# Optimization experiments

Hardware: AMD Instinct MI355X
Metric: run time of the kernel (lower is better)

The kernel has to match this reference:

```python
import math
import jax, jax.numpy as jnp
import numpy as np

NUM_HEADS = 16
INPUT_DIM = 1024
VALUES_DIM = 1024
HEAD_DIM = INPUT_DIM // NUM_HEADS


def _pos_embeddings(length, dim):
    # TENER positional encoding for `length` positions centered at 0: [length, dim]
    half = dim // 2
    position = jnp.arange(-(length // 2), length // 2, dtype=jnp.float32)[:, None]
    div_term = jnp.exp(jnp.arange(half, dtype=jnp.float32) * (-math.log(10000.0) / (half - 1)))
    ang = position * div_term[None, :]
    return jnp.concatenate([jnp.sin(ang), jnp.cos(ang)], axis=1)


def _shift(t):
    # [B,H,S,2S] -> [B,H,S,S] relative-position shift trick
    B, H, S, _ = t.shape
    t = jnp.concatenate([t, jnp.zeros((B, H, S, 1), t.dtype)], axis=-1)  # [B,H,S,2S+1]
    t = t.reshape(B, H, 2 * S + 1, S)[:, :, :-1].reshape(B, H, S, 2 * S)
    return t[..., S:]


def setup_inputs() -> dict:
    key = jax.random.key(0)
    ks = jax.random.split(key, 9)
    B, S, D, Dv = 2, 1024, INPUT_DIM, VALUES_DIM
    s = 1.0 / math.sqrt(D)
    return {
        "query": jax.random.normal(ks[0], (B, S, D), jnp.float32),
        "key": jax.random.normal(ks[1], (B, S, D), jnp.float32),
        "value": jax.random.normal(ks[2], (B, S, D), jnp.float32),
        "mask": jnp.ones((B, S), jnp.int32),
        "Wq": jax.random.normal(ks[3], (D, D), jnp.float32) * s,
        "bq": jnp.zeros((D,), jnp.float32),
        "Wv": jax.random.normal(ks[4], (Dv, D), jnp.float32) * s,
        "bv": jnp.zeros((Dv,), jnp.float32),
        "Wo": jax.random.normal(ks[5], (D, Dv), jnp.float32) * (1.0 / math.sqrt(Dv)),
        "bo": jnp.zeros((D,), jnp.float32),
        "v_bias": jax.random.normal(ks[6], (NUM_HEADS, HEAD_DIM), jnp.float32) * (1.0 / math.sqrt(HEAD_DIM)),
    }


def reference(query, key, value, mask, Wq, bq, Wv, bv, Wo, bo, v_bias):
    B, S, D = query.shape
    H, d = NUM_HEADS, HEAD_DIM
    dv = VALUES_DIM // H
    pos = _pos_embeddings(2 * S, d)  # [2S, d]

    k = key.reshape(B, S, H, d).transpose(0, 2, 1, 3)                       # [B,H,S,d] (no projection!)
    q = (query @ Wq.T + bq).reshape(B, S, H, d).transpose(0, 2, 1, 3)       # [B,H,S,d]
    v = (value @ Wv.T + bv).reshape(B, S, H, dv).transpose(0, 2, 1, 3)      # [B,H,S,dv]

    qk = jnp.einsum('bhqd,bhkd->bhqk', q, k)                                # [B,H,S,S]
    v_bias_rel = jnp.einsum('hd,ld->hl', v_bias, pos)[None, :, None, :]     # [1,H,1,2S]
    q_rel = jnp.einsum('bhqd,ld->bhql', q, pos)                             # [B,H,S,2S]
    rel = _shift(q_rel + v_bias_rel)                                        # [B,H,S,S]

    attn = jax.nn.softmax(qk + rel, axis=-1)                                # unscaled, unmasked (matches source)
    x = jnp.einsum('bhqk,bhkd->bhqd', attn, v)                              # [B,H,S,dv]
    x = x.transpose(0, 2, 1, 3).reshape(B, S, VALUES_DIM)
    return x @ Wo.T + bo
```

## Files before the change

### kernel.cpp

```cpp
#include <hip/hip_runtime.h>
#include <math.h>

#define SEQ 1024
#define DIM 1024
#define NH 16
#define HD 64
#define NB 2

typedef __attribute__((ext_vector_type(8))) short bf16x8;
typedef __attribute__((ext_vector_type(8))) _Float16 f16x8;
typedef __attribute__((ext_vector_type(4))) float f32x4;
typedef __attribute__((ext_vector_type(8))) unsigned short ushort8;
typedef __attribute__((ext_vector_type(4))) unsigned short ushort4v;

#define DT_CONST (-0.2971077539347156f)
#define FIXEDM 32.0f

__device__ __forceinline__ unsigned short f2bf(float x) {
    unsigned u = __float_as_uint(x);
    return (unsigned short)((u + 0x7fffu + ((u >> 16) & 1u)) >> 16);
}
__device__ __forceinline__ float bf2f(unsigned short h) {
    return __uint_as_float(((unsigned)h) << 16);
}
__device__ __forceinline__ unsigned short f2h(float x) {
    _Float16 h = (_Float16)x;
    return __builtin_bit_cast(unsigned short, h);
}

__device__ __forceinline__ void plain8(const float* __restrict__ s,
                                       unsigned short* __restrict__ h, int i) {
    float4 v0 = *(const float4*)&s[i];
    float4 v1 = *(const float4*)&s[i + 4];
    float vs[8] = {v0.x, v0.y, v0.z, v0.w, v1.x, v1.y, v1.z, v1.w};
    ushort8 hv;
    #pragma unroll
    for (int k = 0; k < 8; ++k) hv[k] = f2bf(vs[k]);
    *(ushort8*)&h[i] = hv;
}
__device__ __forceinline__ void plain8h(const float* __restrict__ s,
                                        unsigned short* __restrict__ h, int i) {
    float4 v0 = *(const float4*)&s[i];
    float4 v1 = *(const float4*)&s[i + 4];
    float vs[8] = {v0.x, v0.y, v0.z, v0.w, v1.x, v1.y, v1.z, v1.w};
    ushort8 hv;
    #pragma unroll
    for (int k = 0; k < 8; ++k) hv[k] = f2h(vs[k]);
    *(ushort8*)&h[i] = hv;
}

__global__ __launch_bounds__(256) void conv_all(
    const float* __restrict__ query, const float* __restrict__ key,
    const float* __restrict__ value, const float* __restrict__ Wq,
    const float* __restrict__ Wv, const float* __restrict__ Wo,
    unsigned short* __restrict__ Aqh,
    unsigned short* __restrict__ Khs,
    unsigned short* __restrict__ Vb,
    unsigned short* __restrict__ Wqh,
    unsigned short* __restrict__ Wvh,
    unsigned short* __restrict__ Woh,
    unsigned short* __restrict__ Kth)
{
    int i = (blockIdx.x * 256 + threadIdx.x) * 8;
    int r = blockIdx.y;
    const int NSMALL = DIM * DIM;
    if (r >= 3 && r <= 5 && i >= NSMALL) return;
    if (r == 6 && i >= SEQ * HD) return;
    switch (r) {
        case 0: plain8h(query, Aqh, i); break;
        case 1: plain8h(key,   Khs, i); break;
        case 2: plain8(value, Vb, i); break;
        case 3: plain8h(Wq, Wqh, i); break;
        case 4: plain8(Wv, Wvh, i); break;
        case 5: plain8(Wo, Woh, i); break;
        case 6: {
            ushort8 hv;
            #pragma unroll
            for (int k = 0; k < 8; ++k) {
                int idx = i + k;
                int j = idx >> 6;
                int c = idx & 63;
                int ii = c & 31;
                float dt = __expf((float)ii * DT_CONST);
                float ang = (float)j * dt;
                float val = (c < 32) ? sinf(ang) : cosf(ang);
                hv[k] = f2h(val);
            }
            *(ushort8*)&Kth[i] = hv;
            break;
        }
    }
}

#define QLD 72

__global__ __launch_bounds__(256) void qv_gemm(
    const unsigned short* __restrict__ Aqh, const unsigned short* __restrict__ Wqh,
    const float* __restrict__ bq,
    const unsigned short* __restrict__ Vb, const unsigned short* __restrict__ Wvh,
    const float* __restrict__ bv,
    const float* __restrict__ v_bias,
    unsigned short* __restrict__ Qh,
    unsigned short* __restrict__ vpT)
{
    __shared__ __align__(16) unsigned short smem[192 * QLD];
    unsigned short* sAh = smem;
    unsigned short* sWh = smem + 128 * QLD;

    const int K = DIM;

    int bid = blockIdx.x;
    int s = bid >> 3;
    int y = (bid & 7) + 8 * (s & 1);
    int h = (s >> 1) & 15;
    bool isq = (s >> 5) == 0;
    int m0 = y * 128;
    int n0 = h * 64;

    int tid = threadIdx.x;
    int lane = tid & 63;
    int w = tid >> 6;
    int l16 = lane & 15, quad = lane >> 4;

    int ar = tid >> 2;
    int c0 = (tid & 3) << 3;
    int c1 = c0 + 32;

    const unsigned short* pAh0 = (isq ? Aqh : Vb) + (size_t)(m0 + ar) * K;
    const unsigned short* pAh1 = pAh0 + (size_t)64 * K;
    const unsigned short* pWh  = (isq ? Wqh : Wvh) + (size_t)(n0 + ar) * K;

    f32x4 acc[2][4];
    #pragma unroll
    for (int mq = 0; mq < 2; ++mq)
        #pragma unroll
        for (int nt = 0; nt < 4; ++nt)
            acc[mq][nt] = (f32x4){0.f, 0.f, 0.f, 0.f};

    ushort8 ra[4], rw[2];
    ra[0] = *(const ushort8*)(pAh0 + c0);  ra[1] = *(const ushort8*)(pAh0 + c1);
    ra[2] = *(const ushort8*)(pAh1 + c0);  ra[3] = *(const ushort8*)(pAh1 + c1);
    rw[0] = *(const ushort8*)(pWh + c0);   rw[1] = *(const ushort8*)(pWh + c1);

    for (int kk = 0; kk < K; kk += 64) {
        __syncthreads();
        *(ushort8*)&sAh[ar * QLD + c0] = ra[0];
        *(ushort8*)&sAh[ar * QLD + c1] = ra[1];
        *(ushort8*)&sAh[(ar + 64) * QLD + c0] = ra[2];
        *(ushort8*)&sAh[(ar + 64) * QLD + c1] = ra[3];
        *(ushort8*)&sWh[ar * QLD + c0] = rw[0];
        *(ushort8*)&sWh[ar * QLD + c1] = rw[1];
        if (kk + 64 < K) {
            int kn = kk + 64;
            ra[0] = *(const ushort8*)(pAh0 + kn + c0);  ra[1] = *(const ushort8*)(pAh0 + kn + c1);
            ra[2] = *(const ushort8*)(pAh1 + kn + c0);  ra[3] = *(const ushort8*)(pAh1 + kn + c1);
            rw[0] = *(const ushort8*)(pWh + kn + c0);   rw[1] = *(const ushort8*)(pWh + kn + c1);
        }
        __syncthreads();

        #pragma unroll
        for (int c = 0; c < 2; ++c) {
            int kpos = c * 32 + quad * 8;
            bf16x8 af[2];
            #pragma unroll
            for (int mq = 0; mq < 2; ++mq)
                af[mq] = *(const bf16x8*)&sAh[(w * 32 + mq * 16 + l16) * QLD + kpos];
            bf16x8 bhv[4];
            #pragma unroll
            for (int nt = 0; nt < 4; ++nt)
                bhv[nt] = *(const bf16x8*)&sWh[(nt * 16 + l16) * QLD + kpos];
            if (isq) {
                #pragma unroll
                for (int nt = 0; nt < 4; ++nt)
                    #pragma unroll
                    for (int mq = 0; mq < 2; ++mq)
                        acc[mq][nt] = __builtin_amdgcn_mfma_f32_16x16x32_f16(
                            __builtin_bit_cast(f16x8, af[mq]),
                            __builtin_bit_cast(f16x8, bhv[nt]), acc[mq][nt], 0, 0, 0);
            } else {
                #pragma unroll
                for (int nt = 0; nt < 4; ++nt)
                    #pragma unroll
                    for (int mq = 0; mq < 2; ++mq)
                        acc[mq][nt] = __builtin_amdgcn_mfma_f32_16x16x32_bf16(
                            af[mq], bhv[nt], acc[mq][nt], 0, 0, 0);
            }
        }
    }

    int b = m0 >> 10;

    if (isq) {
        float bql[4], vbs[2], vbc[2], dti[2];
        #pragma unroll
        for (int nt = 0; nt < 4; ++nt) bql[nt] = bq[h * 64 + nt * 16 + l16];
        #pragma unroll
        for (int t = 0; t < 2; ++t) {
            vbs[t] = v_bias[h * 64 + t * 16 + l16];
            vbc[t] = v_bias[h * 64 + 32 + t * 16 + l16];
            dti[t] = __expf((float)(t * 16 + l16) * DT_CONST);
        }
        #pragma unroll
        for (int mq = 0; mq < 2; ++mq) {
            #pragma unroll
            for (int reg = 0; reg < 4; ++reg) {
                int row = m0 + w * 32 + mq * 16 + quad * 4 + reg;
                int q = row & (SEQ - 1);
                size_t qbase = ((size_t)(b * NH + h) * SEQ + q) * 128;
                float hv[4];
                #pragma unroll
                for (int nt = 0; nt < 4; ++nt) hv[nt] = acc[mq][nt][reg] + bql[nt];
                #pragma unroll
                for (int nt = 0; nt < 4; ++nt)
                    Qh[qbase + nt * 16 + l16] = f2h(hv[nt]);
                #pragma unroll
                for (int t = 0; t < 2; ++t) {
                    float u = hv[t] + vbs[t];
                    float wv = hv[t + 2] + vbc[t];
                    float ang = (float)q * dti[t];
                    float C = cosf(ang), S = sinf(ang);
                    float cs = u * C + wv * S;
                    float cc = wv * C - u * S;
                    Qh[qbase + 64 + t * 16 + l16] = f2h(cs);
                    Qh[qbase + 96 + t * 16 + l16] = f2h(cc);
                }
            }
        }
    } else {
        __syncthreads();
        unsigned short* tb = smem;
        #pragma unroll
        for (int nt = 0; nt < 4; ++nt) {
            int d = nt * 16 + l16;
            float bcol = bv[n0 + d];
            #pragma unroll
            for (int mq = 0; mq < 2; ++mq)
                #pragma unroll
                for (int reg = 0; reg < 4; ++reg) {
                    int srow = w * 32 + mq * 16 + quad * 4 + reg;
                    tb[d * 136 + srow] = f2bf(acc[mq][nt][reg] + bcol);
                }
        }
        __syncthreads();
        int s0 = m0 & (SEQ - 1);
        #pragma unroll
        for (int i = tid; i < 1024; i += 256) {
            int dd = i >> 4;
            int j16 = i & 15;
            int sb = j16 >> 3;
            int posl = (j16 & 7) << 3;
            unsigned short tmp[8];
            #pragma unroll
            for (int k = 0; k < 8; ++k) {
                int pos = posl + k;
                int sl = (pos >> 2) + (pos & 3) * 16;
                tmp[k] = tb[dd * 136 + sb * 64 + sl];
            }
            *(ushort8*)&vpT[((size_t)((b * NH + h) * 64 + dd)) * SEQ + s0 + sb * 64 + posl] =
                *(ushort8*)tmp;
        }
    }
}

__global__ __launch_bounds__(256) void out_gemm(
    const unsigned short* __restrict__ Ab, const unsigned short* __restrict__ Woh,
    const float* __restrict__ bo, float* __restrict__ C)
{
    __shared__ __align__(16) unsigned short sA[64 * QLD];
    __shared__ __align__(16) unsigned short sW[64 * QLD];

    const int K = DIM, N = DIM;

    int bid = blockIdx.x;
    int n0 = ((bid >> 3) & 15) * 64;
    int m0 = ((bid & 7) + 8 * (bid >> 7)) * 64;

    int tid = threadIdx.x;
    int lane = tid & 63;
    int w = tid >> 6;
    int l16 = lane & 15, quad = lane >> 4;

    int ar = tid >> 2;
    int c0 = (tid & 3) << 3;
    int c1 = c0 + 32;

    const unsigned short* pA = Ab + (size_t)(m0 + ar) * K;
    const unsigned short* pW = Woh + (size_t)(n0 + ar) * K;

    f32x4 acc[4];
    #pragma unroll
    for (int nt = 0; nt < 4; ++nt) acc[nt] = (f32x4){0.f, 0.f, 0.f, 0.f};

    ushort8 ra[2], rw[2];
    ra[0] = *(const ushort8*)(pA + c0);  ra[1] = *(const ushort8*)(pA + c1);
    rw[0] = *(const ushort8*)(pW + c0);  rw[1] = *(const ushort8*)(pW + c1);

    for (int kk = 0; kk < K; kk += 64) {
        __syncthreads();
        *(ushort8*)&sA[ar * QLD + c0] = ra[0];
        *(ushort8*)&sA[ar * QLD + c1] = ra[1];
        *(ushort8*)&sW[ar * QLD + c0] = rw[0];
        *(ushort8*)&sW[ar * QLD + c1] = rw[1];
        if (kk + 64 < K) {
            int kn = kk + 64;
            ra[0] = *(const ushort8*)(pA + kn + c0);  ra[1] = *(const ushort8*)(pA + kn + c1);
            rw[0] = *(const ushort8*)(pW + kn + c0);  rw[1] = *(const ushort8*)(pW + kn + c1);
        }
        __syncthreads();

        #pragma unroll
        for (int c = 0; c < 2; ++c) {
            int kpos = c * 32 + quad * 8;
            bf16x8 af = *(const bf16x8*)&sA[(w * 16 + l16) * QLD + kpos];
            #pragma unroll
            for (int nt = 0; nt < 4; ++nt) {
                bf16x8 bh = *(const bf16x8*)&sW[(nt * 16 + l16) * QLD + kpos];
                acc[nt] = __builtin_amdgcn_mfma_f32_16x16x32_bf16(af, bh, acc[nt], 0, 0, 0);
            }
        }
    }

    #pragma unroll
    for (int nt = 0; nt < 4; ++nt) {
        int col = n0 + nt * 16 + l16;
        float bcol = bo[col];
        #pragma unroll
        for (int reg = 0; reg < 4; ++reg) {
            int row = m0 + w * 16 + quad * 4 + reg;
            C[(size_t)row * N + col] = acc[nt][reg] + bcol;
        }
    }
}

#define LDK 136
#define LDV 72

__global__ __launch_bounds__(256) void attn_mfma(
    const unsigned short* __restrict__ Kh,
    const unsigned short* __restrict__ vpT,
    const unsigned short* __restrict__ Qh,
    const unsigned short* __restrict__ Kth,
    unsigned short* __restrict__ Opart,
    float* __restrict__ lsum)
{
    __shared__ unsigned short Ksh[64][LDK];
    __shared__ unsigned short Vt[64][LDV];
    __shared__ unsigned short Ps[128][LDV];

    int tid = threadIdx.x;
    int w = tid >> 6;
    int lane = tid & 63;
    int l16 = lane & 15;
    int quad = lane >> 4;

    int bid = blockIdx.x;
    int g = bid & 63;
    int qt = bid >> 6;
    int h = g & 15;
    int b = (g >> 4) & 1;
    int sp = g >> 5;
    int q0 = qt << 7;
    int jb = sp << 3;

    int sr0 = tid >> 3, sp0 = (tid & 7) << 3;
    int sr1 = sr0 + 32;

    ushort8 pK0, pK1, pT0, pT1, pV0, pV1;
    {
        int j0 = jb << 6;
        size_t g0 = (size_t)(b * SEQ + j0 + sr0) * DIM + h * HD + sp0;
        size_t g1 = (size_t)(b * SEQ + j0 + sr1) * DIM + h * HD + sp0;
        pK0 = *(const ushort8*)&Kh[g0]; pK1 = *(const ushort8*)&Kh[g1];
        size_t t0 = (size_t)(j0 + sr0) * 64 + sp0, t1 = (size_t)(j0 + sr1) * 64 + sp0;
        pT0 = *(const ushort8*)&Kth[t0]; pT1 = *(const ushort8*)&Kth[t1];
        size_t v0 = ((size_t)((b * NH + h) * 64 + sr0)) * SEQ + j0 + sp0;
        size_t v1 = ((size_t)((b * NH + h) * 64 + sr1)) * SEQ + j0 + sp0;
        pV0 = *(const ushort8*)&vpT[v0]; pV1 = *(const ushort8*)&vpT[v1];
    }

    bf16x8 ah[2][4];
    #pragma unroll
    for (int half = 0; half < 2; ++half) {
        const unsigned short* gq = Qh + (((size_t)(b * NH + h)) * SEQ + q0 + half * 64) * 128;
        #pragma unroll
        for (int c = tid; c < 1024; c += 256) {
            int r = c >> 4, p = (c & 15) << 3;
            *(ushort8*)&Ksh[r][p] = *(const ushort8*)&gq[r * 128 + p];
        }
        __syncthreads();
        if ((w >> 1) == half) {
            #pragma unroll
            for (int mq = 0; mq < 2; ++mq)
                #pragma unroll
                for (int c = 0; c < 4; ++c)
                    ah[mq][c] = *(const bf16x8*)&Ksh[(w & 1) * 32 + mq * 16 + l16][c * 32 + quad * 8];
        }
        __syncthreads();
    }

    f32x4 oacc[2][4];
    f32x4 lacc[2];
    #pragma unroll
    for (int mq = 0; mq < 2; ++mq) {
        #pragma unroll
        for (int nb = 0; nb < 4; ++nb) oacc[mq][nb] = (f32x4){0.f, 0.f, 0.f, 0.f};
        lacc[mq] = (f32x4){0.f, 0.f, 0.f, 0.f};
    }

    bf16x8 onesv;
    #pragma unroll
    for (int k = 0; k < 8; ++k) onesv[k] = (short)0x3F80;

    for (int jt = 0; jt < 8; ++jt) {
        __syncthreads();
        *(ushort8*)&Ksh[sr0][sp0] = pK0;       *(ushort8*)&Ksh[sr1][sp0] = pK1;
        *(ushort8*)&Ksh[sr0][64 + sp0] = pT0;  *(ushort8*)&Ksh[sr1][64 + sp0] = pT1;
        *(ushort8*)&Vt[sr0][sp0] = pV0;        *(ushort8*)&Vt[sr1][sp0] = pV1;
        if (jt < 7) {
            int j0n = (jb + jt + 1) << 6;
            size_t g0 = (size_t)(b * SEQ + j0n + sr0) * DIM + h * HD + sp0;
            size_t g1 = (size_t)(b * SEQ + j0n + sr1) * DIM + h * HD + sp0;
            pK0 = *(const ushort8*)&Kh[g0]; pK1 = *(const ushort8*)&Kh[g1];
            size_t t0 = (size_t)(j0n + sr0) * 64 + sp0, t1 = (size_t)(j0n + sr1) * 64 + sp0;
            pT0 = *(const ushort8*)&Kth[t0]; pT1 = *(const ushort8*)&Kth[t1];
            size_t v0 = ((size_t)((b * NH + h) * 64 + sr0)) * SEQ + j0n + sp0;
            size_t v1 = ((size_t)((b * NH + h) * 64 + sr1)) * SEQ + j0n + sp0;
            pV0 = *(const ushort8*)&vpT[v0]; pV1 = *(const ushort8*)&vpT[v1];
        }
        __syncthreads();

        f32x4 sacc[2][4];
        #pragma unroll
        for (int mq = 0; mq < 2; ++mq)
            #pragma unroll
            for (int nb = 0; nb < 4; ++nb) sacc[mq][nb] = (f32x4){0.f, 0.f, 0.f, 0.f};
        #pragma unroll
        for (int nb = 0; nb < 4; ++nb) {
            #pragma unroll
            for (int c = 0; c < 4; ++c) {
                bf16x8 bh = *(const bf16x8*)&Ksh[nb * 16 + l16][c * 32 + quad * 8];
                #pragma unroll
                for (int mq = 0; mq < 2; ++mq)
                    sacc[mq][nb] = __builtin_amdgcn_mfma_f32_16x16x32_f16(
                        __builtin_bit_cast(f16x8, ah[mq][c]),
                        __builtin_bit_cast(f16x8, bh), sacc[mq][nb], 0, 0, 0);
            }
        }

        #pragma unroll
        for (int mq = 0; mq < 2; ++mq) {
            #pragma unroll
            for (int r = 0; r < 4; ++r) {
                float p0 = __expf(sacc[mq][0][r] - FIXEDM);
                float p1 = __expf(sacc[mq][1][r] - FIXEDM);
                float p2 = __expf(sacc[mq][2][r] - FIXEDM);
                float p3 = __expf(sacc[mq][3][r] - FIXEDM);
                int prow = w * 32 + mq * 16 + quad * 4 + r;
                ushort4v pv4;
                pv4.x = f2bf(p0); pv4.y = f2bf(p1); pv4.z = f2bf(p2); pv4.w = f2bf(p3);
                *(ushort4v*)&Ps[prow][l16 * 4] = pv4;
            }
        }
        __syncthreads();

        #pragma unroll
        for (int kc = 0; kc < 2; ++kc) {
            bf16x8 a[2];
            #pragma unroll
            for (int mq = 0; mq < 2; ++mq) {
                a[mq] = *(const bf16x8*)&Ps[w * 32 + mq * 16 + l16][kc * 32 + quad * 8];
                lacc[mq] = __builtin_amdgcn_mfma_f32_16x16x32_bf16(a[mq], onesv, lacc[mq], 0, 0, 0);
            }
            #pragma unroll
            for (int nb = 0; nb < 4; ++nb) {
                bf16x8 bv = *(const bf16x8*)&Vt[nb * 16 + l16][kc * 32 + quad * 8];
                #pragma unroll
                for (int mq = 0; mq < 2; ++mq)
                    oacc[mq][nb] = __builtin_amdgcn_mfma_f32_16x16x32_bf16(a[mq], bv, oacc[mq][nb], 0, 0, 0);
            }
        }
    }

    const size_t OOFF = (size_t)sp * NB * NH * SEQ * 64;
    const size_t LOFF = (size_t)sp * NB * NH * SEQ;
    #pragma unroll
    for (int mq = 0; mq < 2; ++mq) {
        #pragma unroll
        for (int r = 0; r < 4; ++r) {
            int qrow = q0 + w * 32 + mq * 16 + quad * 4 + r;
            size_t rowi = (size_t)(b * NH + h) * SEQ + qrow;
            #pragma unroll
            for (int nb = 0; nb < 4; ++nb)
                Opart[OOFF + rowi * 64 + nb * 16 + l16] = f2bf(oacc[mq][nb][r]);
            if (l16 == 0)
                lsum[LOFF + rowi] = lacc[mq][r];
        }
    }
}

__global__ __launch_bounds__(256) void attn_combine(
    const unsigned short* __restrict__ Opart, const float* __restrict__ lsum,
    unsigned short* __restrict__ xab)
{
    const size_t OOFF = (size_t)NB * NH * SEQ * 64;
    const size_t LOFF = (size_t)NB * NH * SEQ;
    int tid = threadIdx.x;
    int d = tid & 63;
    size_t r = (size_t)blockIdx.x * 4 + (tid >> 6);
    int q = (int)(r & (SEQ - 1));
    int h = (int)((r >> 10) & (NH - 1));
    int b = (int)(r >> 14);

    float inv = 1.f / (lsum[r] + lsum[LOFF + r]);
    float O0 = bf2f(Opart[r * 64 + d]);
    float O1 = bf2f(Opart[OOFF + r * 64 + d]);
    float o = (O0 + O1) * inv;
    xab[((size_t)(b * SEQ + q)) * DIM + h * HD + d] = f2bf(o);
}

extern "C" void kernel_launch(void* const* d_in, const int* in_sizes, int n_in,
                              void* d_out, int out_size, void* d_ws, size_t ws_size,
                              hipStream_t stream) {
    const float* query  = (const float*)d_in[0];
    const float* key    = (const float*)d_in[1];
    const float* value  = (const float*)d_in[2];
    const float* Wq     = (const float*)d_in[4];
    const float* bq     = (const float*)d_in[5];
    const float* Wv     = (const float*)d_in[6];
    const float* bv     = (const float*)d_in[7];
    const float* Wo     = (const float*)d_in[8];
    const float* bo     = (const float*)d_in[9];
    const float* v_bias = (const float*)d_in[10];

    float* out = (float*)d_out;
    char* base = (char*)d_ws;
    const size_t MB = 1024 * 1024;

    unsigned short* Aqh   = (unsigned short*)(base);
    unsigned short* vpT   = (unsigned short*)(base +  4 * MB);
    unsigned short* Khs   = (unsigned short*)(base +  8 * MB);
    unsigned short* Qh    = (unsigned short*)(base + 12 * MB);
    unsigned short* Wqh   = (unsigned short*)(base + 20 * MB);
    unsigned short* Vb    = (unsigned short*)(base + 22 * MB);
    unsigned short* Wvh   = (unsigned short*)(base + 26 * MB);
    unsigned short* Woh   = (unsigned short*)(base + 28 * MB);
    unsigned short* Kth   = (unsigned short*)(base + 30 * MB);
    unsigned short* xab   = (unsigned short*)(base + 31 * MB);
    float*          lsum  = (float*)(base + 35 * MB);
    unsigned short* Opart = (unsigned short*)(base + 36 * MB);

    const int M = NB * SEQ;

    dim3 cgrid(M * DIM / 2048, 7);
    conv_all<<<cgrid, 256, 0, stream>>>(query, key, value, Wq, Wv, Wo,
                                        Aqh, Khs, Vb, Wqh, Wvh, Woh, Kth);

    qv_gemm<<<512, 256, 0, stream>>>(Aqh, Wqh, bq, Vb, Wvh, bv,
                                     v_bias, Qh, vpT);

    attn_mfma<<<512, 256, 0, stream>>>(Khs, vpT, Qh, Kth, Opart, lsum);

    attn_combine<<<NB * NH * SEQ / 4, 256, 0, stream>>>(Opart, lsum, xab);

    out_gemm<<<512, 256, 0, stream>>>(xab, Woh, bo, out);
}
```

Before: 157.4 us.

## Shrink QV GEMM tile to 64 rows and simplify block-index mappings

The QV projection GEMM moves from 128x64 tiles to 64x64 tiles on a 3D grid of 1024 blocks, which halves the shared memory and accumulator footprint per block. The out_gemm and attention kernels drop their swizzled block-to-tile mappings in favour of plain linear or 2D grid indexing. The smaller tiles should raise occupancy and parallelism, at the cost of re-reading the weight tiles more often. The plain mappings may also give up whatever L2 locality the earlier swizzle provided.

```diff
diff --git a/kernel.cpp b/kernel.cpp
--- a/kernel.cpp
+++ b/kernel.cpp
@@ -103,68 +103,53 @@
     unsigned short* __restrict__ Qh,
     unsigned short* __restrict__ vpT)
 {
-    __shared__ __align__(16) unsigned short smem[192 * QLD];
+    __shared__ __align__(16) unsigned short smem[128 * QLD];
     unsigned short* sAh = smem;
-    unsigned short* sWh = smem + 128 * QLD;
+    unsigned short* sWh = smem + 64 * QLD;
 
     const int K = DIM;
-
-    int bid = blockIdx.x;
-    int s = bid >> 3;
-    int y = (bid & 7) + 8 * (s & 1);
-    int h = (s >> 1) & 15;
-    bool isq = (s >> 5) == 0;
-    int m0 = y * 128;
-    int n0 = h * 64;
+    bool isq = (blockIdx.z == 0);
 
     int tid = threadIdx.x;
     int lane = tid & 63;
     int w = tid >> 6;
     int l16 = lane & 15, quad = lane >> 4;
+    int m0 = blockIdx.y * 64;
+    int h = blockIdx.x;
+    int n0 = h * 64;
 
     int ar = tid >> 2;
     int c0 = (tid & 3) << 3;
     int c1 = c0 + 32;
 
-    const unsigned short* pAh0 = (isq ? Aqh : Vb) + (size_t)(m0 + ar) * K;
-    const unsigned short* pAh1 = pAh0 + (size_t)64 * K;
-    const unsigned short* pWh  = (isq ? Wqh : Wvh) + (size_t)(n0 + ar) * K;
-
-    f32x4 acc[2][4];
-    #pragma unroll
-    for (int mq = 0; mq < 2; ++mq)
-        #pragma unroll
-        for (int nt = 0; nt < 4; ++nt)
-            acc[mq][nt] = (f32x4){0.f, 0.f, 0.f, 0.f};
-
-    ushort8 ra[4], rw[2];
-    ra[0] = *(const ushort8*)(pAh0 + c0);  ra[1] = *(const ushort8*)(pAh0 + c1);
-    ra[2] = *(const ushort8*)(pAh1 + c0);  ra[3] = *(const ushort8*)(pAh1 + c1);
-    rw[0] = *(const ushort8*)(pWh + c0);   rw[1] = *(const ushort8*)(pWh + c1);
+    const unsigned short* pAh = (isq ? Aqh : Vb) + (size_t)(m0 + ar) * K;
+    const unsigned short* pWh = (isq ? Wqh : Wvh) + (size_t)(n0 + ar) * K;
+
+    f32x4 acc[4];
+    #pragma unroll
+    for (int nt = 0; nt < 4; ++nt) acc[nt] = (f32x4){0.f, 0.f, 0.f, 0.f};
+
+    ushort8 ra[2], rw[2];
+    ra[0] = *(const ushort8*)(pAh + c0);  ra[1] = *(const ushort8*)(pAh + c1);
+    rw[0] = *(const ushort8*)(pWh + c0);  rw[1] = *(const ushort8*)(pWh + c1);
 
     for (int kk = 0; kk < K; kk += 64) {
         __syncthreads();
         *(ushort8*)&sAh[ar * QLD + c0] = ra[0];
         *(ushort8*)&sAh[ar * QLD + c1] = ra[1];
-        *(ushort8*)&sAh[(ar + 64) * QLD + c0] = ra[2];
-        *(ushort8*)&sAh[(ar + 64) * QLD + c1] = ra[3];
         *(ushort8*)&sWh[ar * QLD + c0] = rw[0];
         *(ushort8*)&sWh[ar * QLD + c1] = rw[1];
         if (kk + 64 < K) {
             int kn = kk + 64;
-            ra[0] = *(const ushort8*)(pAh0 + kn + c0);  ra[1] = *(const ushort8*)(pAh0 + kn + c1);
-            ra[2] = *(const ushort8*)(pAh1 + kn + c0);  ra[3] = *(const ushort8*)(pAh1 + kn + c1);
-            rw[0] = *(const ushort8*)(pWh + kn + c0);   rw[1] = *(const ushort8*)(pWh + kn + c1);
+            ra[0] = *(const ushort8*)(pAh + kn + c0);  ra[1] = *(const ushort8*)(pAh + kn + c1);
+            rw[0] = *(const ushort8*)(pWh + kn + c0);  rw[1] = *(const ushort8*)(pWh + kn + c1);
         }
         __syncthreads();
 
         #pragma unroll
         for (int c = 0; c < 2; ++c) {
             int kpos = c * 32 + quad * 8;
-            bf16x8 af[2];
-            #pragma unroll
-            for (int mq = 0; mq < 2; ++mq)
-                af[mq] = *(const bf16x8*)&sAh[(w * 32 + mq * 16 + l16) * QLD + kpos];
+            bf16x8 af = *(const bf16x8*)&sAh[(w * 16 + l16) * QLD + kpos];
             bf16x8 bhv[4];
             #pragma unroll
             for (int nt = 0; nt < 4; ++nt)
@@ -172,18 +157,14 @@
             if (isq) {
                 #pragma unroll
                 for (int nt = 0; nt < 4; ++nt)
-                    #pragma unroll
-                    for (int mq = 0; mq < 2; ++mq)
-                        acc[mq][nt] = __builtin_amdgcn_mfma_f32_16x16x32_f16(
-                            __builtin_bit_cast(f16x8, af[mq]),
-                            __builtin_bit_cast(f16x8, bhv[nt]), acc[mq][nt], 0, 0, 0);
+                    acc[nt] = __builtin_amdgcn_mfma_f32_16x16x32_f16(
+                        __builtin_bit_cast(f16x8, af),
+                        __builtin_bit_cast(f16x8, bhv[nt]), acc[nt], 0, 0, 0);
             } else {
                 #pragma unroll
                 for (int nt = 0; nt < 4; ++nt)
-                    #pragma unroll
-                    for (int mq = 0; mq < 2; ++mq)
-                        acc[mq][nt] = __builtin_amdgcn_mfma_f32_16x16x32_bf16(
-                            af[mq], bhv[nt], acc[mq][nt], 0, 0, 0);
+                    acc[nt] = __builtin_amdgcn_mfma_f32_16x16x32_bf16(
+                        af, bhv[nt], acc[nt], 0, 0, 0);
             }
         }
     }
@@ -201,29 +182,26 @@
             dti[t] = __expf((float)(t * 16 + l16) * DT_CONST);
         }
         #pragma unroll
-        for (int mq = 0; mq < 2; ++mq) {
-            #pragma unroll
-            for (int reg = 0; reg < 4; ++reg) {
-                int row = m0 + w * 32 + mq * 16 + quad * 4 + reg;
-                int q = row & (SEQ - 1);
-                size_t qbase = ((size_t)(b * NH + h) * SEQ + q) * 128;
-                float hv[4];
-                #pragma unroll
-                for (int nt = 0; nt < 4; ++nt) hv[nt] = acc[mq][nt][reg] + bql[nt];
-                #pragma unroll
-                for (int nt = 0; nt < 4; ++nt)
-                    Qh[qbase + nt * 16 + l16] = f2h(hv[nt]);
-                #pragma unroll
-                for (int t = 0; t < 2; ++t) {
-                    float u = hv[t] + vbs[t];
-                    float wv = hv[t + 2] + vbc[t];
-                    float ang = (float)q * dti[t];
-                    float C = cosf(ang), S = sinf(ang);
-                    float cs = u * C + wv * S;
-                    float cc = wv * C - u * S;
-                    Qh[qbase + 64 + t * 16 + l16] = f2h(cs);
-                    Qh[qbase + 96 + t * 16 + l16] = f2h(cc);
-                }
+        for (int reg = 0; reg < 4; ++reg) {
+            int row = m0 + w * 16 + quad * 4 + reg;
+            int q = row & (SEQ - 1);
+            size_t qbase = ((size_t)(b * NH + h) * SEQ + q) * 128;
+            float hv[4];
+            #pragma unroll
+            for (int nt = 0; nt < 4; ++nt) hv[nt] = acc[nt][reg] + bql[nt];
+            #pragma unroll
+            for (int nt = 0; nt < 4; ++nt)
+                Qh[qbase + nt * 16 + l16] = f2h(hv[nt]);
+            #pragma unroll
+            for (int t = 0; t < 2; ++t) {
+                float u = hv[t] + vbs[t];
+                float wv = hv[t + 2] + vbc[t];
+                float ang = (float)q * dti[t];
+                float C = cosf(ang), S = sinf(ang);
+                float cs = u * C + wv * S;
+                float cc = wv * C - u * S;
+                Qh[qbase + 64 + t * 16 + l16] = f2h(cs);
+                Qh[qbase + 96 + t * 16 + l16] = f2h(cc);
             }
         }
     } else {
@@ -234,29 +212,26 @@
             int d = nt * 16 + l16;
             float bcol = bv[n0 + d];
             #pragma unroll
-            for (int mq = 0; mq < 2; ++mq)
-                #pragma unroll
-                for (int reg = 0; reg < 4; ++reg) {
-                    int srow = w * 32 + mq * 16 + quad * 4 + reg;
-                    tb[d * 136 + srow] = f2bf(acc[mq][nt][reg] + bcol);
-                }
+            for (int reg = 0; reg < 4; ++reg) {
+                int srow = w * 16 + quad * 4 + reg;
+                tb[d * 136 + srow] = f2bf(acc[nt][reg] + bcol);
+            }
         }
         __syncthreads();
         int s0 = m0 & (SEQ - 1);
         #pragma unroll
-        for (int i = tid; i < 1024; i += 256) {
-            int dd = i >> 4;
-            int j16 = i & 15;
-            int sb = j16 >> 3;
-            int posl = (j16 & 7) << 3;
+        for (int i = tid; i < 512; i += 256) {
+            int dd = i >> 3;
+            int j8 = i & 7;
+            int posl = j8 << 3;
             unsigned short tmp[8];
             #pragma unroll
             for (int k = 0; k < 8; ++k) {
                 int pos = posl + k;
                 int sl = (pos >> 2) + (pos & 3) * 16;
-                tmp[k] = tb[dd * 136 + sb * 64 + sl];
-            }
-            *(ushort8*)&vpT[((size_t)((b * NH + h) * 64 + dd)) * SEQ + s0 + sb * 64 + posl] =
+                tmp[k] = tb[dd * 136 + sl];
+            }
+            *(ushort8*)&vpT[((size_t)((b * NH + h) * 64 + dd)) * SEQ + s0 + posl] =
                 *(ushort8*)tmp;
         }
     }
@@ -271,9 +246,7 @@
 
     const int K = DIM, N = DIM;
 
-    int bid = blockIdx.x;
-    int n0 = ((bid >> 3) & 15) * 64;
-    int m0 = ((bid & 7) + 8 * (bid >> 7)) * 64;
+    int m0 = blockIdx.y * 64, n0 = blockIdx.x * 64;
 
     int tid = threadIdx.x;
     int lane = tid & 63;
@@ -354,11 +327,10 @@
     int quad = lane >> 4;
 
     int bid = blockIdx.x;
-    int g = bid & 63;
-    int qt = bid >> 6;
-    int h = g & 15;
-    int b = (g >> 4) & 1;
-    int sp = g >> 5;
+    int qt = bid & 7;
+    int h = (bid >> 3) & 15;
+    int b = (bid >> 7) & 1;
+    int sp = bid >> 8;
     int q0 = qt << 7;
     int jb = sp << 3;
 
@@ -555,12 +527,15 @@
     conv_all<<<cgrid, 256, 0, stream>>>(query, key, value, Wq, Wv, Wo,
                                         Aqh, Khs, Vb, Wqh, Wvh, Woh, Kth);
 
-    qv_gemm<<<512, 256, 0, stream>>>(Aqh, Wqh, bq, Vb, Wvh, bv,
-                                     v_bias, Qh, vpT);
-
-    attn_mfma<<<512, 256, 0, stream>>>(Khs, vpT, Qh, Kth, Opart, lsum);
+    dim3 qvgrid(NH, M / 64, 2);
+    qv_gemm<<<qvgrid, 256, 0, stream>>>(Aqh, Wqh, bq, Vb, Wvh, bv,
+                                        v_bias, Qh, vpT);
+
+    attn_mfma<<<2 * NB * NH * (SEQ / 128), 256, 0, stream>>>(Khs, vpT, Qh,
+                                                             Kth, Opart, lsum);
 
     attn_combine<<<NB * NH * SEQ / 4, 256, 0, stream>>>(Opart, lsum, xab);
 
-    out_gemm<<<512, 256, 0, stream>>>(xab, Woh, bo, out);
-}
+    dim3 ogrid(DIM / 64, M / 64);
+    out_gemm<<<ogrid, 256, 0, stream>>>(xab, Woh, bo, out);
+}
```

Measured after the change: 160.2 us. Within noise of the previous version (+1.8%).

## Use lighter LDS-only barriers and simpler block-to-tile mappings

Applied to the files above, without the earlier changes.

Replaces __syncthreads with a custom barrier that waits only on LDS counters (lgkmcnt) before s_barrier. This lets outstanding global prefetch loads stay in flight across the barrier. It also reverts the swizzled blockIdx-to-tile mappings in the GEMMs and attention kernel to straightforward 2D/3D grids and ordering, which changes L2 locality and CU scheduling. The risk is that the barrier no longer orders global memory, and the new block ordering may reduce cache reuse.

```diff
diff --git a/kernel.cpp b/kernel.cpp
--- a/kernel.cpp
+++ b/kernel.cpp
@@ -26,6 +26,12 @@
 __device__ __forceinline__ unsigned short f2h(float x) {
     _Float16 h = (_Float16)x;
     return __builtin_bit_cast(unsigned short, h);
+}
+
+__device__ __forceinline__ void wg_barrier() {
+    asm volatile("s_waitcnt lgkmcnt(0)" ::: "memory");
+    __builtin_amdgcn_s_barrier();
+    asm volatile("" ::: "memory");
 }
 
 __device__ __forceinline__ void plain8(const float* __restrict__ s,
@@ -108,19 +114,15 @@
     unsigned short* sWh = smem + 128 * QLD;
 
     const int K = DIM;
-
-    int bid = blockIdx.x;
-    int s = bid >> 3;
-    int y = (bid & 7) + 8 * (s & 1);
-    int h = (s >> 1) & 15;
-    bool isq = (s >> 5) == 0;
-    int m0 = y * 128;
-    int n0 = h * 64;
+    bool isq = (blockIdx.z == 0);
 
     int tid = threadIdx.x;
     int lane = tid & 63;
     int w = tid >> 6;
     int l16 = lane & 15, quad = lane >> 4;
+    int m0 = blockIdx.y * 128;
+    int h = blockIdx.x;
+    int n0 = h * 64;
 
     int ar = tid >> 2;
     int c0 = (tid & 3) << 3;
@@ -143,7 +145,7 @@
     rw[0] = *(const ushort8*)(pWh + c0);   rw[1] = *(const ushort8*)(pWh + c1);
 
     for (int kk = 0; kk < K; kk += 64) {
-        __syncthreads();
+        wg_barrier();
         *(ushort8*)&sAh[ar * QLD + c0] = ra[0];
         *(ushort8*)&sAh[ar * QLD + c1] = ra[1];
         *(ushort8*)&sAh[(ar + 64) * QLD + c0] = ra[2];
@@ -156,7 +158,7 @@
             ra[2] = *(const ushort8*)(pAh1 + kn + c0);  ra[3] = *(const ushort8*)(pAh1 + kn + c1);
             rw[0] = *(const ushort8*)(pWh + kn + c0);   rw[1] = *(const ushort8*)(pWh + kn + c1);
         }
-        __syncthreads();
+        wg_barrier();
 
         #pragma unroll
         for (int c = 0; c < 2; ++c) {
@@ -271,9 +273,7 @@
 
     const int K = DIM, N = DIM;
 
-    int bid = blockIdx.x;
-    int n0 = ((bid >> 3) & 15) * 64;
-    int m0 = ((bid & 7) + 8 * (bid >> 7)) * 64;
+    int m0 = blockIdx.y * 64, n0 = blockIdx.x * 64;
 
     int tid = threadIdx.x;
     int lane = tid & 63;
@@ -296,7 +296,7 @@
     rw[0] = *(const ushort8*)(pW + c0);  rw[1] = *(const ushort8*)(pW + c1);
 
     for (int kk = 0; kk < K; kk += 64) {
-        __syncthreads();
+        wg_barrier();
         *(ushort8*)&sA[ar * QLD + c0] = ra[0];
         *(ushort8*)&sA[ar * QLD + c1] = ra[1];
         *(ushort8*)&sW[ar * QLD + c0] = rw[0];
@@ -306,7 +306,7 @@
             ra[0] = *(const ushort8*)(pA + kn + c0);  ra[1] = *(const ushort8*)(pA + kn + c1);
             rw[0] = *(const ushort8*)(pW + kn + c0);  rw[1] = *(const ushort8*)(pW + kn + c1);
         }
-        __syncthreads();
+        wg_barrier();
 
         #pragma unroll
         for (int c = 0; c < 2; ++c) {
@@ -354,11 +354,10 @@
     int quad = lane >> 4;
 
     int bid = blockIdx.x;
-    int g = bid & 63;
-    int qt = bid >> 6;
-    int h = g & 15;
-    int b = (g >> 4) & 1;
-    int sp = g >> 5;
+    int qt = bid & 7;
+    int h = (bid >> 3) & 15;
+    int b = (bid >> 7) & 1;
+    int sp = bid >> 8;
     int q0 = qt << 7;
     int jb = sp << 3;
 
@@ -387,7 +386,7 @@
             int r = c >> 4, p = (c & 15) << 3;
             *(ushort8*)&Ksh[r][p] = *(const ushort8*)&gq[r * 128 + p];
         }
-        __syncthreads();
+        wg_barrier();
         if ((w >> 1) == half) {
             #pragma unroll
             for (int mq = 0; mq < 2; ++mq)
@@ -395,7 +394,7 @@
                 for (int c = 0; c < 4; ++c)
                     ah[mq][c] = *(const bf16x8*)&Ksh[(w & 1) * 32 + mq * 16 + l16][c * 32 + quad * 8];
         }
-        __syncthreads();
+        wg_barrier();
     }
 
     f32x4 oacc[2][4];
@@ -412,7 +411,7 @@
     for (int k = 0; k < 8; ++k) onesv[k] = (short)0x3F80;
 
     for (int jt = 0; jt < 8; ++jt) {
-        __syncthreads();
+        wg_barrier();
         *(ushort8*)&Ksh[sr0][sp0] = pK0;       *(ushort8*)&Ksh[sr1][sp0] = pK1;
         *(ushort8*)&Ksh[sr0][64 + sp0] = pT0;  *(ushort8*)&Ksh[sr1][64 + sp0] = pT1;
         *(ushort8*)&Vt[sr0][sp0] = pV0;        *(ushort8*)&Vt[sr1][sp0] = pV1;
@@ -427,7 +426,7 @@
             size_t v1 = ((size_t)((b * NH + h) * 64 + sr1)) * SEQ + j0n + sp0;
             pV0 = *(const ushort8*)&vpT[v0]; pV1 = *(const ushort8*)&vpT[v1];
         }
-        __syncthreads();
+        wg_barrier();
 
         f32x4 sacc[2][4];
         #pragma unroll
@@ -461,7 +460,7 @@
                 *(ushort4v*)&Ps[prow][l16 * 4] = pv4;
             }
         }
-        __syncthreads();
+        wg_barrier();
 
         #pragma unroll
         for (int kc = 0; kc < 2; ++kc) {
@@ -555,12 +554,15 @@
     conv_all<<<cgrid, 256, 0, stream>>>(query, key, value, Wq, Wv, Wo,
                                         Aqh, Khs, Vb, Wqh, Wvh, Woh, Kth);
 
-    qv_gemm<<<512, 256, 0, stream>>>(Aqh, Wqh, bq, Vb, Wvh, bv,
-                                     v_bias, Qh, vpT);
-
-    attn_mfma<<<512, 256, 0, stream>>>(Khs, vpT, Qh, Kth, Opart, lsum);
+    dim3 qvgrid(NH, M / 128, 2);
+    qv_gemm<<<qvgrid, 256, 0, stream>>>(Aqh, Wqh, bq, Vb, Wvh, bv,
+                                        v_bias, Qh, vpT);
+
+    attn_mfma<<<2 * NB * NH * (SEQ / 128), 256, 0, stream>>>(Khs, vpT, Qh,
+                                                             Kth, Opart, lsum);
 
     attn_combine<<<NB * NH * SEQ / 4, 256, 0, stream>>>(Opart, lsum, xab);
 
-    out_gemm<<<512, 256, 0, stream>>>(xab, Woh, bo, out);
-}
+    dim3 ogrid(DIM / 64, M / 64);
+    out_gemm<<<ogrid, 256, 0, stream>>>(xab, Woh, bo, out);
+}
```

After: 158.1 us. No clear change (+0.5%).
